# Kernel optimization log

Measured on AMD Instinct MI355X. Metric: run time of the kernel, lower is better.

## Reference

```python
import jax, jax.numpy as jnp
import numpy as np
import math

D_MODEL = 1024
NUM_HEADS = 16
HEAD_DIM = D_MODEL // NUM_HEADS  # 64
PLANE_DIM = HEAD_DIM // 2        # 32
ROPE_THETA = 10000.0
ROPE_PERIOD = 1024.0
ROPE_SCALE = 2.0 * math.pi / ROPE_PERIOD


def _inv_freq():
    # 1 / theta^(arange(0, plane_dim, 2)/plane_dim)  -> [plane_dim//2] = [16]
    return 1.0 / ROPE_THETA ** (jnp.arange(0, PLANE_DIM, 2, dtype=jnp.float32) / PLANE_DIM)


def _rotate_pairs(x, sin, cos):
    # x: [B,H,N,P], sin/cos: [B,1,N,P//2]
    x0 = x[..., 0::2]
    x1 = x[..., 1::2]
    y0 = x0 * cos - x1 * sin
    y1 = x0 * sin + x1 * cos
    return jnp.stack([y0, y1], axis=-1).reshape(x.shape)


def _apply_rope_2d(x, pos_2d, inv_freq):
    # x: [B,H,N,D], pos_2d: [B,N,2]
    ang_x = pos_2d[..., 0] * ROPE_SCALE  # [B,N]
    ang_y = pos_2d[..., 1] * ROPE_SCALE
    fx = ang_x[..., None] * inv_freq     # [B,N,P//2]
    fy = ang_y[..., None] * inv_freq
    sin_x, cos_x = jnp.sin(fx)[:, None], jnp.cos(fx)[:, None]  # [B,1,N,P//2]
    sin_y, cos_y = jnp.sin(fy)[:, None], jnp.cos(fy)[:, None]
    xp, yp = x[..., :PLANE_DIM], x[..., PLANE_DIM:]
    xp = _rotate_pairs(xp, sin_x, cos_x)
    yp = _rotate_pairs(yp, sin_y, cos_y)
    return jnp.concatenate([xp, yp], axis=-1)


def setup_inputs() -> dict:
    key = jax.random.key(0)
    ks = jax.random.split(key, 12)
    B, N, d = 2, 2048, D_MODEL
    s = 1.0 / math.sqrt(d)
    return {
        "x": jax.random.normal(ks[0], (B, N, d), jnp.float32),
        "q_positions": jax.random.uniform(ks[1], (B, N, 2), jnp.float32) * ROPE_PERIOD,
        "kv_positions": jax.random.uniform(ks[2], (B, N, 2), jnp.float32) * ROPE_PERIOD,
        "Wq": jax.random.normal(ks[3], (d, d), jnp.float32) * s,
        "bq": jnp.zeros((d,), jnp.float32),
        "Wk": jax.random.normal(ks[4], (d, d), jnp.float32) * s,
        "bk": jnp.zeros((d,), jnp.float32),
        "Wv": jax.random.normal(ks[5], (d, d), jnp.float32) * s,
        "bv": jnp.zeros((d,), jnp.float32),
        "Wo": jax.random.normal(ks[6], (d, d), jnp.float32) * s,
        "bo": jnp.zeros((d,), jnp.float32),
    }


def reference(x, q_positions, kv_positions, Wq, bq, Wk, bk, Wv, bv, Wo, bo):
    B, Nq, _ = x.shape
    H, D = NUM_HEADS, HEAD_DIM
    inv_freq = _inv_freq()
    # fused-style QKV projections (torch Linear: x @ W.T + b)
    q = (jnp.einsum('bnd,od->bno', x, Wq) + bq).reshape(B, Nq, H, D).transpose(0, 2, 1, 3)
    k = (jnp.einsum('bnd,od->bno', x, Wk) + bk).reshape(B, Nq, H, D).transpose(0, 2, 1, 3)
    v = (jnp.einsum('bnd,od->bno', x, Wv) + bv).reshape(B, Nq, H, D).transpose(0, 2, 1, 3)
    q = _apply_rope_2d(q, q_positions, inv_freq)
    k = _apply_rope_2d(k, kv_positions, inv_freq)
    logits = jnp.einsum('bhqd,bhkd->bhqk', q, k) / math.sqrt(D)
    attn = jax.nn.softmax(logits, axis=-1)
    out = jnp.einsum('bhqk,bhkd->bhqd', attn, v)
    out = out.transpose(0, 2, 1, 3).reshape(B, Nq, D_MODEL)
    return jnp.einsum('bnd,od->bno', out, Wo) + bo
```

## Files before the change

### kernel.cpp

```cpp
#include <hip/hip_runtime.h>
#include <math.h>

#define SEQ   2048
#define DM    1024
#define NTOK  4096
#define HEADS 16
#define HDIM  64
#define ROPE_SCALE 0.006135923151542565f
#define L2_10000   13.287712379549449f

typedef __attribute__((ext_vector_type(8))) short bf16x8;
typedef __attribute__((ext_vector_type(4))) unsigned short u16x4;
typedef __attribute__((ext_vector_type(4))) float f32x4;

__device__ __forceinline__ unsigned short f2bf(float f) {
    unsigned int u = __float_as_uint(f);
    return (unsigned short)((u + 0x7FFFu + ((u >> 16) & 1u)) >> 16);
}
__device__ __forceinline__ float bf2f(unsigned short h) {
    return __uint_as_float(((unsigned int)h) << 16);
}

__device__ __forceinline__ void split8(const float* __restrict__ src, bf16x8& h, bf16x8& l) {
    float4 f0 = ((const float4*)src)[0];
    float4 f1 = ((const float4*)src)[1];
    float fv[8] = {f0.x,f0.y,f0.z,f0.w,f1.x,f1.y,f1.z,f1.w};
    #pragma unroll
    for (int j = 0; j < 8; ++j) {
        unsigned short hb = f2bf(fv[j]);
        h[j] = (short)hb;
        l[j] = (short)f2bf(fv[j] - bf2f(hb));
    }
}

__device__ __forceinline__ void gload16(const void* g, void* l) {
    __builtin_amdgcn_global_load_lds(
        (const __attribute__((address_space(1))) unsigned int*)g,
        (__attribute__((address_space(3))) unsigned int*)l, 16, 0, 0);
}

__global__ __launch_bounds__(256) void pack_swz(
    const float* __restrict__ src, unsigned short* __restrict__ dst)
{
    const int idx = blockIdx.x*256 + threadIdx.x;
    const int e = idx * 8;
    const int r = e >> 10, k0 = e & 1023;
    bf16x8 h, l;
    split8(src + (size_t)r*DM + k0, h, l);
    const int mt = r >> 7, rl = r & 127;
    const int kt = k0 >> 5, kl = k0 & 31;
    char* tb = (char*)(dst + ((size_t)(mt*32 + kt))*8192);
    const int sw = (rl & 7) << 4;
    *(bf16x8*)(tb + ((rl*128 + kl*2) ^ sw))      = h;
    *(bf16x8*)(tb + ((rl*128 + 64 + kl*2) ^ sw)) = l;
}

__global__ __launch_bounds__(256) void pack_swz3(
    const float* __restrict__ Wq, const float* __restrict__ Wk,
    const float* __restrict__ Wv, unsigned short* __restrict__ dst)
{
    const int idx = blockIdx.x*256 + threadIdx.x;
    const int e = idx * 8;
    const int r = e >> 10, k0 = e & 1023;
    const int proj = r >> 10;
    const float* W = proj==0 ? Wq : (proj==1 ? Wk : Wv);
    bf16x8 h, l;
    split8(W + (size_t)(r & 1023)*DM + k0, h, l);
    const int mt = r >> 7, rl = r & 127;
    const int kt = k0 >> 5, kl = k0 & 31;
    char* tb = (char*)(dst + ((size_t)(mt*32 + kt))*8192);
    const int sw = (rl & 7) << 4;
    *(bf16x8*)(tb + ((rl*128 + kl*2) ^ sw))      = h;
    *(bf16x8*)(tb + ((rl*128 + 64 + kl*2) ^ sw)) = l;
}

__global__ __launch_bounds__(256, 3) void gemm_mfma(
    const unsigned short* __restrict__ Ap, const unsigned short* __restrict__ Bp,
    const int mode,
    const float* __restrict__ bq, const float* __restrict__ bk,
    const float* __restrict__ bv,
    const float* __restrict__ qpos, const float* __restrict__ kpos,
    unsigned short* __restrict__ qo, unsigned short* __restrict__ ko,
    unsigned short* __restrict__ vo,
    const float* __restrict__ bo, float* __restrict__ outp)
{
    __shared__ __align__(16) unsigned short Ab[8192];
    __shared__ __align__(16) unsigned short Bb[8192];

    const int tid = threadIdx.x, lane = tid & 63, wv = tid >> 6;
    const int col = lane & 15, grp = lane >> 4;
    const int wr = wv >> 1, wc = wv & 1;

    const int NX = gridDim.x, NB = NX * gridDim.y;
    const int bid = blockIdx.y * NX + blockIdx.x;
    const int bid2 = (bid & 7) * (NB >> 3) + (bid >> 3);
    const int nt = bid2 % NX, mt = bid2 / NX;

    f32x4 acc[4][4];
    #pragma unroll
    for (int mf=0; mf<4; ++mf)
        #pragma unroll
        for (int nf=0; nf<4; ++nf)
            acc[mf][nf] = (f32x4)0.f;

    for (int kt = 0; kt < 32; ++kt) {
        __syncthreads();
        {
            const char* ga = (const char*)Ap + ((size_t)(mt*32 + kt))*16384;
            const char* gb = (const char*)Bp + ((size_t)(nt*32 + kt))*16384;
            #pragma unroll
            for (int rep = 0; rep < 4; ++rep) {
                const int o = wv*4096 + rep*1024;
                gload16(ga + o + lane*16, (char*)Ab + o);
                gload16(gb + o + lane*16, (char*)Bb + o);
            }
        }
        __syncthreads();
        const char* A = (const char*)Ab;
        const char* B = (const char*)Bb;
        bf16x8 ah[4], al[4];
        #pragma unroll
        for (int mf = 0; mf < 4; ++mf) {
            const int rl = wr*64 + mf*16 + col;
            const int b0 = rl*128 + grp*16;
            const int sw = (rl & 7) << 4;
            ah[mf] = *(const bf16x8*)(A + (b0 ^ sw));
            al[mf] = *(const bf16x8*)(A + ((b0 + 64) ^ sw));
        }
        #pragma unroll
        for (int nf = 0; nf < 4; ++nf) {
            const int rl = wc*64 + nf*16 + col;
            const int b0 = rl*128 + grp*16;
            const int sw = (rl & 7) << 4;
            bf16x8 bh  = *(const bf16x8*)(B + (b0 ^ sw));
            bf16x8 blo = *(const bf16x8*)(B + ((b0 + 64) ^ sw));
            #pragma unroll
            for (int mf = 0; mf < 4; ++mf) {
                acc[mf][nf] = __builtin_amdgcn_mfma_f32_16x16x32_bf16(ah[mf], bh,  acc[mf][nf], 0,0,0);
                acc[mf][nf] = __builtin_amdgcn_mfma_f32_16x16x32_bf16(ah[mf], blo, acc[mf][nf], 0,0,0);
                acc[mf][nf] = __builtin_amdgcn_mfma_f32_16x16x32_bf16(al[mf], bh,  acc[mf][nf], 0,0,0);
            }
        }
    }

    const int m0 = mt*128, n0 = nt*128;
    if (mode == 1) {
        #pragma unroll
        for (int nf = 0; nf < 4; ++nf) {
            const int n = n0 + wc*64 + nf*16 + col;
            const float bn = bo[n];
            #pragma unroll
            for (int mf = 0; mf < 4; ++mf)
                #pragma unroll
                for (int i = 0; i < 4; ++i) {
                    const int tok = m0 + wr*64 + mf*16 + grp*4 + i;
                    outp[(size_t)tok*DM + n] = acc[mf][nf][i] + bn;
                }
        }
    } else {
        const int proj = n0 >> 10;
        const float* bb = proj==0 ? bq : (proj==1 ? bk : bv);
        unsigned short* op = proj==0 ? qo : (proj==1 ? ko : vo);
        const float* pp = proj==0 ? qpos : kpos;
        #pragma unroll
        for (int nf = 0; nf < 4; ++nf) {
            const int n  = n0 + wc*64 + nf*16 + col;
            const int nn = n & 1023;
            const int h  = nn >> 6, dd = nn & 63;
            const float bn = bb[nn];
            if (proj == 2) {
                #pragma unroll
                for (int mf = 0; mf < 4; ++mf) {
                    const int tok0 = m0 + wr*64 + mf*16 + grp*4;
                    const int b = tok0 >> 11, sq0 = tok0 & 2047;
                    u16x4 h4, l4;
                    #pragma unroll
                    for (int i = 0; i < 4; ++i) {
                        const float val = acc[mf][nf][i] + bn;
                        unsigned short hb = f2bf(val);
                        h4[i] = hb;
                        l4[i] = f2bf(val - bf2f(hb));
                    }
                    const int bh2 = (b*HEADS + h)*2;
                    *(u16x4*)(op + ((size_t)(bh2+0)*HDIM + dd)*SEQ + sq0) = h4;
                    *(u16x4*)(op + ((size_t)(bh2+1)*HDIM + dd)*SEQ + sq0) = l4;
                }
            } else {
                const int plane = dd >> 5;
                const float e = (float)(dd & 30) * (1.0f/32.0f);
                const float invf = exp2f(-L2_10000 * e);
                #pragma unroll
                for (int mf = 0; mf < 4; ++mf)
                    #pragma unroll
                    for (int i = 0; i < 4; ++i) {
                        const int tok = m0 + wr*64 + mf*16 + grp*4 + i;
                        const int b = tok >> 11, sq = tok & 2047;
                        const float pv = pp[((size_t)(b*SEQ + sq))*2 + plane];
                        const float ang = pv * ROPE_SCALE * invf;
                        float s, c;
                        sincosf(ang, &s, &c);
                        const float val = acc[mf][nf][i] + bn;
                        const float prt = __shfl_xor(val, 1);
                        const float res = (dd & 1) ? (prt*s + val*c) : (val*c - prt*s);
                        unsigned short hb = f2bf(res);
                        unsigned short lb = f2bf(res - bf2f(hb));
                        const int bh2 = (b*HEADS + h)*2;
                        op[((size_t)(bh2+0)*SEQ + sq)*HDIM + dd] = hb;
                        op[((size_t)(bh2+1)*SEQ + sq)*HDIM + dd] = lb;
                    }
            }
        }
    }
}

#define KB 32

__global__ __launch_bounds__(256) void attn_mfma(
    const unsigned short* __restrict__ q, const unsigned short* __restrict__ k,
    const unsigned short* __restrict__ v, float* __restrict__ ao)
{
    const int bh  = blockIdx.y;
    const int qb0 = blockIdx.x * 128;
    const int tid = threadIdx.x;
    const int lane = tid & 63;
    const int wv   = tid >> 6;
    const int col  = lane & 15;
    const int grp  = lane >> 4;

    __shared__ __align__(16) unsigned short Khi[KB][72];
    __shared__ __align__(16) unsigned short Klo[KB][72];
    __shared__ __align__(16) unsigned short Vthi[HDIM][40];
    __shared__ __align__(16) unsigned short Vtlo[HDIM][40];
    __shared__ __align__(16) unsigned short Pb[4][32][40];

    const unsigned short* kh_g = k + (size_t)(bh*2)*SEQ*HDIM;
    const unsigned short* kl_g = kh_g + (size_t)SEQ*HDIM;
    const unsigned short* vh_g = v + (size_t)(bh*2)*HDIM*SEQ;
    const unsigned short* vl_g = vh_g + (size_t)HDIM*SEQ;

    bf16x8 qhi[2][2], qlo[2][2];
    {
        const unsigned short* qh_g = q + (size_t)(bh*2)*SEQ*HDIM;
        const unsigned short* ql_g = qh_g + (size_t)SEQ*HDIM;
        #pragma unroll
        for (int mf = 0; mf < 2; ++mf)
            #pragma unroll
            for (int ks = 0; ks < 2; ++ks) {
                const size_t off = (size_t)(qb0 + wv*32 + mf*16 + col)*HDIM + ks*32 + grp*8;
                qhi[mf][ks] = *(const bf16x8*)(qh_g + off);
                qlo[mf][ks] = *(const bf16x8*)(ql_g + off);
            }
    }

    f32x4 o[2][4];
    #pragma unroll
    for (int mf=0; mf<2; ++mf)
        #pragma unroll
        for (int nf=0; nf<4; ++nf)
            o[mf][nf] = (f32x4)0.f;
    float mrun[2][4], lrun[2][4];
    #pragma unroll
    for (int mf=0; mf<2; ++mf)
        #pragma unroll
        for (int r=0; r<4; ++r) { mrun[mf][r] = -INFINITY; lrun[mf][r] = 0.f; }

    for (int kt = 0; kt < SEQ; kt += KB) {
        __syncthreads();
        {
            const int row = tid >> 3, c0 = (tid & 7) * 8;
            const size_t off = (size_t)(kt + row)*HDIM + c0;
            *(bf16x8*)&Khi[row][c0] = *(const bf16x8*)(kh_g + off);
            *(bf16x8*)&Klo[row][c0] = *(const bf16x8*)(kl_g + off);
        }
        {
            const int d = tid >> 2, c = (tid & 3) * 8;
            const size_t off = (size_t)d*SEQ + kt + c;
            *(bf16x8*)&Vthi[d][c] = *(const bf16x8*)(vh_g + off);
            *(bf16x8*)&Vtlo[d][c] = *(const bf16x8*)(vl_g + off);
        }
        __syncthreads();

        f32x4 s[2][2];
        #pragma unroll
        for (int mf=0; mf<2; ++mf)
            #pragma unroll
            for (int nf=0; nf<2; ++nf)
                s[mf][nf] = (f32x4)0.f;
        #pragma unroll
        for (int ks = 0; ks < 2; ++ks) {
            bf16x8 kh[2], kl[2];
            #pragma unroll
            for (int nf = 0; nf < 2; ++nf) {
                kh[nf] = *(const bf16x8*)&Khi[nf*16 + col][ks*32 + grp*8];
                kl[nf] = *(const bf16x8*)&Klo[nf*16 + col][ks*32 + grp*8];
            }
            #pragma unroll
            for (int mf = 0; mf < 2; ++mf)
                #pragma unroll
                for (int nf = 0; nf < 2; ++nf) {
                    s[mf][nf] = __builtin_amdgcn_mfma_f32_16x16x32_bf16(qhi[mf][ks], kh[nf], s[mf][nf], 0,0,0);
                    s[mf][nf] = __builtin_amdgcn_mfma_f32_16x16x32_bf16(qlo[mf][ks], kh[nf], s[mf][nf], 0,0,0);
                    s[mf][nf] = __builtin_amdgcn_mfma_f32_16x16x32_bf16(qhi[mf][ks], kl[nf], s[mf][nf], 0,0,0);
                }
        }

        #pragma unroll
        for (int mf=0; mf<2; ++mf)
            #pragma unroll
            for (int nf=0; nf<2; ++nf)
                s[mf][nf] *= 0.125f;

        #pragma unroll
        for (int mf = 0; mf < 2; ++mf) {
            #pragma unroll
            for (int r = 0; r < 4; ++r) {
                float m2 = fmaxf(s[mf][0][r], s[mf][1][r]);
                m2 = fmaxf(m2, __shfl_xor(m2, 1, 16));
                m2 = fmaxf(m2, __shfl_xor(m2, 2, 16));
                m2 = fmaxf(m2, __shfl_xor(m2, 4, 16));
                m2 = fmaxf(m2, __shfl_xor(m2, 8, 16));
                const float mnew = fmaxf(mrun[mf][r], m2);
                const float corr = __expf(mrun[mf][r] - mnew);
                mrun[mf][r] = mnew;
                const float p0 = __expf(s[mf][0][r] - mnew);
                const float p1 = __expf(s[mf][1][r] - mnew);
                float ts = p0 + p1;
                ts += __shfl_xor(ts, 1, 16);
                ts += __shfl_xor(ts, 2, 16);
                ts += __shfl_xor(ts, 4, 16);
                ts += __shfl_xor(ts, 8, 16);
                lrun[mf][r] = lrun[mf][r]*corr + ts;
                #pragma unroll
                for (int nf=0; nf<4; ++nf) o[mf][nf][r] *= corr;
                Pb[wv][mf*16 + grp*4 + r][col]      = f2bf(p0);
                Pb[wv][mf*16 + grp*4 + r][16 + col] = f2bf(p1);
            }
        }

        bf16x8 pa[2];
        #pragma unroll
        for (int mf=0; mf<2; ++mf)
            pa[mf] = *(const bf16x8*)&Pb[wv][mf*16 + col][grp*8];
        #pragma unroll
        for (int nf = 0; nf < 4; ++nf) {
            bf16x8 vh = *(const bf16x8*)&Vthi[nf*16 + col][grp*8];
            bf16x8 vl = *(const bf16x8*)&Vtlo[nf*16 + col][grp*8];
            #pragma unroll
            for (int mf = 0; mf < 2; ++mf) {
                o[mf][nf] = __builtin_amdgcn_mfma_f32_16x16x32_bf16(pa[mf], vh, o[mf][nf], 0,0,0);
                o[mf][nf] = __builtin_amdgcn_mfma_f32_16x16x32_bf16(pa[mf], vl, o[mf][nf], 0,0,0);
            }
        }
    }

    const int b = bh >> 4, h = bh & 15;
    #pragma unroll
    for (int mf = 0; mf < 2; ++mf)
        #pragma unroll
        for (int r = 0; r < 4; ++r) {
            const float inv = 1.0f / lrun[mf][r];
            const int n = qb0 + wv*32 + mf*16 + grp*4 + r;
            float* orow = ao + (((size_t)b*SEQ + n)*HEADS + h)*HDIM;
            #pragma unroll
            for (int nf = 0; nf < 4; ++nf)
                orow[nf*16 + col] = o[mf][nf][r] * inv;
        }
}

extern "C" void kernel_launch(void* const* d_in, const int* in_sizes, int n_in,
                              void* d_out, int out_size, void* d_ws, size_t ws_size,
                              hipStream_t stream)
{
    const float* x    = (const float*)d_in[0];
    const float* qpos = (const float*)d_in[1];
    const float* kpos = (const float*)d_in[2];
    const float* Wq   = (const float*)d_in[3];
    const float* bq   = (const float*)d_in[4];
    const float* Wk   = (const float*)d_in[5];
    const float* bk   = (const float*)d_in[6];
    const float* Wv   = (const float*)d_in[7];
    const float* bv   = (const float*)d_in[8];
    const float* Wo   = (const float*)d_in[9];
    const float* bo   = (const float*)d_in[10];
    float* out = (float*)d_out;

    unsigned short* qp = (unsigned short*)d_ws;
    unsigned short* kp = qp + (size_t)8388608;
    unsigned short* vp = kp + (size_t)8388608;
    unsigned short* Xp = vp + (size_t)8388608;
    float*          aw = (float*)Xp;
    unsigned short* Wqkvp = Xp + (size_t)8388608;
    unsigned short* Wop   = Wqkvp + (size_t)6291456;
    unsigned short* Ap2   = qp;

    pack_swz <<<2048, 256, 0, stream>>>(x, Xp);
    pack_swz3<<<1536, 256, 0, stream>>>(Wq, Wk, Wv, Wqkvp);
    pack_swz <<< 512, 256, 0, stream>>>(Wo, Wop);

    gemm_mfma<<<dim3(24, 32), 256, 0, stream>>>(
        Xp, Wqkvp, 0, bq, bk, bv, qpos, kpos, qp, kp, vp, nullptr, nullptr);

    attn_mfma<<<dim3(SEQ/128, 2*HEADS), 256, 0, stream>>>(qp, kp, vp, aw);

    pack_swz <<<2048, 256, 0, stream>>>(aw, Ap2);

    gemm_mfma<<<dim3(8, 32), 256, 0, stream>>>(
        Ap2, Wop, 1, nullptr, nullptr, nullptr, nullptr, nullptr,
        nullptr, nullptr, nullptr, bo, out);
}
```

Before: 666.3 us.

## Enlarge GEMM block tile to 256x128 with 512 threads sharing B tile

The projection GEMM now uses 512-thread blocks covering 256 rows by 128 columns. Eight waves share one staged B tile, and the A tile in LDS is doubled. This halves the grid in M and cuts redundant B loads from global memory per output element. In exchange each block uses more LDS (48KB), launch bounds now request 6 waves-per-EU-equivalent occupancy that may pressure registers, and there are fewer blocks to spread over the CUs.

```diff
diff --git a/kernel.cpp b/kernel.cpp
--- a/kernel.cpp
+++ b/kernel.cpp
@@ -9,9 +9,9 @@
 #define ROPE_SCALE 0.006135923151542565f
 #define L2_10000   13.287712379549449f
 
-typedef __attribute__((ext_vector_type(8))) short bf16x8;
-typedef __attribute__((ext_vector_type(4))) unsigned short u16x4;
-typedef __attribute__((ext_vector_type(4))) float f32x4;
+typedef __attribute__((ext_vector_type(8)))  short bf16x8;
+typedef __attribute__((ext_vector_type(4)))  unsigned short u16x4;
+typedef __attribute__((ext_vector_type(4)))  float f32x4;
 
 __device__ __forceinline__ unsigned short f2bf(float f) {
     unsigned int u = __float_as_uint(f);
@@ -74,7 +74,7 @@
     *(bf16x8*)(tb + ((rl*128 + 64 + kl*2) ^ sw)) = l;
 }
 
-__global__ __launch_bounds__(256, 3) void gemm_mfma(
+__global__ __launch_bounds__(512, 6) void gemm_mfma(
     const unsigned short* __restrict__ Ap, const unsigned short* __restrict__ Bp,
     const int mode,
     const float* __restrict__ bq, const float* __restrict__ bk,
@@ -84,12 +84,12 @@
     unsigned short* __restrict__ vo,
     const float* __restrict__ bo, float* __restrict__ outp)
 {
-    __shared__ __align__(16) unsigned short Ab[8192];
+    __shared__ __align__(16) unsigned short Ab[16384];
     __shared__ __align__(16) unsigned short Bb[8192];
 
     const int tid = threadIdx.x, lane = tid & 63, wv = tid >> 6;
     const int col = lane & 15, grp = lane >> 4;
-    const int wr = wv >> 1, wc = wv & 1;
+    const int wr = wv >> 1, wn = wv & 1;
 
     const int NX = gridDim.x, NB = NX * gridDim.y;
     const int bid = blockIdx.y * NX + blockIdx.x;
@@ -106,13 +106,20 @@
     for (int kt = 0; kt < 32; ++kt) {
         __syncthreads();
         {
-            const char* ga = (const char*)Ap + ((size_t)(mt*32 + kt))*16384;
-            const char* gb = (const char*)Bp + ((size_t)(nt*32 + kt))*16384;
             #pragma unroll
             for (int rep = 0; rep < 4; ++rep) {
                 const int o = wv*4096 + rep*1024;
-                gload16(ga + o + lane*16, (char*)Ab + o);
-                gload16(gb + o + lane*16, (char*)Bb + o);
+                const int th = o >> 14, inner = o & 16383;
+                const char* g = (const char*)Ap
+                    + ((size_t)((mt*2 + th)*32 + kt))*16384 + inner;
+                gload16(g + lane*16, (char*)Ab + o);
+            }
+            #pragma unroll
+            for (int rep = 0; rep < 2; ++rep) {
+                const int o = wv*2048 + rep*1024;
+                const char* g = (const char*)Bp
+                    + ((size_t)(nt*32 + kt))*16384 + o;
+                gload16(g + lane*16, (char*)Bb + o);
             }
         }
         __syncthreads();
@@ -122,14 +129,15 @@
         #pragma unroll
         for (int mf = 0; mf < 4; ++mf) {
             const int rl = wr*64 + mf*16 + col;
-            const int b0 = rl*128 + grp*16;
-            const int sw = (rl & 7) << 4;
-            ah[mf] = *(const bf16x8*)(A + (b0 ^ sw));
-            al[mf] = *(const bf16x8*)(A + ((b0 + 64) ^ sw));
+            const int th = rl >> 7, r7 = rl & 127;
+            const int b0 = r7*128 + grp*16;
+            const int sw = (r7 & 7) << 4;
+            ah[mf] = *(const bf16x8*)(A + th*16384 + (b0 ^ sw));
+            al[mf] = *(const bf16x8*)(A + th*16384 + ((b0 + 64) ^ sw));
         }
         #pragma unroll
         for (int nf = 0; nf < 4; ++nf) {
-            const int rl = wc*64 + nf*16 + col;
+            const int rl = wn*64 + nf*16 + col;
             const int b0 = rl*128 + grp*16;
             const int sw = (rl & 7) << 4;
             bf16x8 bh  = *(const bf16x8*)(B + (b0 ^ sw));
@@ -143,11 +151,11 @@
         }
     }
 
-    const int m0 = mt*128, n0 = nt*128;
+    const int m0 = mt*256, n0 = nt*128;
     if (mode == 1) {
         #pragma unroll
         for (int nf = 0; nf < 4; ++nf) {
-            const int n = n0 + wc*64 + nf*16 + col;
+            const int n = n0 + wn*64 + nf*16 + col;
             const float bn = bo[n];
             #pragma unroll
             for (int mf = 0; mf < 4; ++mf)
@@ -164,7 +172,7 @@
         const float* pp = proj==0 ? qpos : kpos;
         #pragma unroll
         for (int nf = 0; nf < 4; ++nf) {
-            const int n  = n0 + wc*64 + nf*16 + col;
+            const int n  = n0 + wn*64 + nf*16 + col;
             const int nn = n & 1023;
             const int h  = nn >> 6, dd = nn & 63;
             const float bn = bb[nn];
@@ -397,14 +405,14 @@
     pack_swz3<<<1536, 256, 0, stream>>>(Wq, Wk, Wv, Wqkvp);
     pack_swz <<< 512, 256, 0, stream>>>(Wo, Wop);
 
-    gemm_mfma<<<dim3(24, 32), 256, 0, stream>>>(
+    gemm_mfma<<<dim3(24, 16), 512, 0, stream>>>(
         Xp, Wqkvp, 0, bq, bk, bv, qpos, kpos, qp, kp, vp, nullptr, nullptr);
 
     attn_mfma<<<dim3(SEQ/128, 2*HEADS), 256, 0, stream>>>(qp, kp, vp, aw);
 
     pack_swz <<<2048, 256, 0, stream>>>(aw, Ap2);
 
-    gemm_mfma<<<dim3(8, 32), 256, 0, stream>>>(
+    gemm_mfma<<<dim3(8, 16), 512, 0, stream>>>(
         Ap2, Wop, 1, nullptr, nullptr, nullptr, nullptr, nullptr,
         nullptr, nullptr, nullptr, bo, out);
 }
```

After: 1.687 ms. +153.2%, slower.
